# Kernel optimization log

Measured on AMD Instinct MI355X. Metric: run time of the kernel, lower is better.

Reference implementation:

```python
import jax, jax.numpy as jnp
import numpy as np

NUM_GROUPS = 32
EPS = 1e-6


def group_norm(x, gamma, beta):
    # x: [b, c, t, h, w]
    b, c, t, h, w = x.shape
    xg = x.reshape(b, NUM_GROUPS, c // NUM_GROUPS, t, h, w)
    mean = xg.mean(axis=(2, 3, 4, 5), keepdims=True)
    var = xg.var(axis=(2, 3, 4, 5), keepdims=True)
    xg = (xg - mean) * jax.lax.rsqrt(var + EPS)
    xn = xg.reshape(b, c, t, h, w)
    return xn * gamma[None, :, None, None, None] + beta[None, :, None, None, None]


def conv1x1(x, w, bias):
    # 1x1x1 Conv3d == per-position channel matmul. x: [b,c,t,h,w], w: [cout,cin]
    y = jnp.einsum('oc,bcthw->bothw', w, x)
    return y + bias[None, :, None, None, None]


def setup_inputs() -> dict:
    key = jax.random.key(0)
    ks = jax.random.split(key, 11)
    c = 512
    b, t, h, w = 1, 16, 32, 32
    s = 1.0 / np.sqrt(c)
    return {
        'x': jax.random.normal(ks[0], (b, c, t, h, w), dtype=jnp.float32),
        'gn_gamma': jnp.ones((c,), jnp.float32),
        'gn_beta': jnp.zeros((c,), jnp.float32),
        'wq': jax.random.normal(ks[1], (c, c), jnp.float32) * s,
        'bq': jnp.zeros((c,), jnp.float32),
        'wk': jax.random.normal(ks[2], (c, c), jnp.float32) * s,
        'bk': jnp.zeros((c,), jnp.float32),
        'wv': jax.random.normal(ks[3], (c, c), jnp.float32) * s,
        'bv': jnp.zeros((c,), jnp.float32),
        'wo': jax.random.normal(ks[4], (c, c), jnp.float32) * s,
        'bo': jnp.zeros((c,), jnp.float32),
    }


def reference(x, gn_gamma, gn_beta, wq, bq, wk, bk, wv, bv, wo, bo):
    b, c, t, h, w = x.shape
    h_ = group_norm(x, gn_gamma, gn_beta)
    q = conv1x1(h_, wq, bq)
    k = conv1x1(h_, wk, bk)
    v = conv1x1(h_, wv, bv)
    # per-frame spatial attention: tokens are the h*w grid, batched over (b t)
    n = h * w
    q = q.transpose(0, 2, 3, 4, 1).reshape(b * t, n, c)   # [(bt), n, c]
    k = k.transpose(0, 2, 3, 4, 1).reshape(b * t, n, c)
    v = v.transpose(0, 2, 3, 4, 1).reshape(b * t, n, c)
    scale = float(int(c) ** (-0.5))
    attn = jax.nn.softmax(jnp.einsum('bic,bjc->bij', q, k) * scale, axis=-1)
    out = jnp.einsum('bij,bjc->bic', attn, v)             # [(bt), n, c]
    out = out.reshape(b, t, h, w, c).transpose(0, 4, 1, 2, 3)
    out = conv1x1(out, wo, bo)
    return x + out
```

## Files before the change

### kernel.cpp

```cpp
#include <hip/hip_runtime.h>
#include <hip/hip_bf16.h>

#define CCH   512
#define NPOS  16384
#define NTOK  1024
#define NFRM  16
#define NGRP  32
#define GSZ   (CCH / NGRP)
#define GELEM (GSZ * NPOS)
#define GN_SPLIT 32

typedef unsigned short u16;
typedef unsigned int   u32;
typedef __attribute__((ext_vector_type(8))) short  short8;
typedef __attribute__((ext_vector_type(4))) float  floatx4;

__device__ __forceinline__ float bf2f(u16 u) {
    return __uint_as_float(((u32)u) << 16);
}
__device__ __forceinline__ u16 f2bf(float f) {
    u32 u = __float_as_uint(f);
    u = (u + 0x7fffu + ((u >> 16) & 1u)) >> 16;
    return (u16)u;
}
__device__ __forceinline__ float ldx(const void* p, size_t i, bool f32m) {
    return f32m ? ((const float*)p)[i] : bf2f(((const u16*)p)[i]);
}
__device__ __forceinline__ void gl2lds16(const u16* g, u16* l) {
    __builtin_amdgcn_global_load_lds(
        (const __attribute__((address_space(1))) u32*)g,
        (__attribute__((address_space(3))) u32*)l, 16, 0, 0);
}

__device__ __forceinline__ bool calc_f32m(const u32* __restrict__ x32) {
    __shared__ int cnt;
    if (threadIdx.x == 0) cnt = 0;
    __syncthreads();
    int c = 0;
    for (int i = threadIdx.x; i < 4096; i += 256) {
        u32 v = x32[i] & 0xFFFFu;
        u32 e = (v >> 7) & 0xFFu;
        if (e >= 0xC8u) c++;
    }
    atomicAdd(&cnt, c);
    __syncthreads();
    return cnt > 64;
}

__launch_bounds__(256)
__global__ void prep_all(const void* __restrict__ x,
                         const void* w0, const void* w1, const void* w2, const void* w3,
                         const void* b0, const void* b1, const void* b2, const void* b3,
                         u16* __restrict__ wdst, u16* __restrict__ bdst,
                         float* __restrict__ rl, float2* __restrict__ partials,
                         u32* __restrict__ flag) {
    int b = blockIdx.x;
    if (b >= 1025 && b < 1089) {
        rl[(b - 1025) * 256 + threadIdx.x] = 0.0f;
        return;
    }
    bool f32m = calc_f32m((const u32*)x);
    if (b == 0 && threadIdx.x == 0) *flag = f32m ? 1u : 0u;

    if (b < 1024) {
        int wi = b >> 8;
        const void* src = (wi == 0) ? w0 : (wi == 1) ? w1 : (wi == 2) ? w2 : w3;
        int base = (b & 255) * 1024 + threadIdx.x * 4;
        u16* d = wdst + wi * 262144 + base;
        if (f32m) {
            float4 v = *(const float4*)((const float*)src + base);
            ushort4 o;
            o.x = f2bf(v.x); o.y = f2bf(v.y); o.z = f2bf(v.z); o.w = f2bf(v.w);
            *(ushort4*)d = o;
        } else {
            *(ushort4*)d = *(const ushort4*)((const u16*)src + base);
        }
    } else if (b == 1024) {
        int t = threadIdx.x;
        int bi = t >> 6;
        int off = (t & 63) * 8;
        const void* src = (bi == 0) ? b0 : (bi == 1) ? b1 : (bi == 2) ? b2 : b3;
        u16* d = bdst + bi * 512 + off;
        if (f32m) {
            float4 v1 = *(const float4*)((const float*)src + off);
            float4 v2 = *(const float4*)((const float*)src + off + 4);
            ushort4 o1, o2;
            o1.x = f2bf(v1.x); o1.y = f2bf(v1.y); o1.z = f2bf(v1.z); o1.w = f2bf(v1.w);
            o2.x = f2bf(v2.x); o2.y = f2bf(v2.y); o2.z = f2bf(v2.z); o2.w = f2bf(v2.w);
            *(ushort4*)d = o1; *(ushort4*)(d + 4) = o2;
        } else {
            *(ushort4*)d = *(const ushort4*)((const u16*)src + off);
            *(ushort4*)(d + 4) = *(const ushort4*)((const u16*)src + off + 4);
        }
    } else {
        __shared__ float sm[8];
        int bb = b - 1089;
        const int chunk = GELEM / GN_SPLIT;
        size_t base = (size_t)bb * chunk;
        float s = 0.f, ss = 0.f;
        if (f32m) {
            const float4* p = (const float4*)((const float*)x + base);
            for (int i = threadIdx.x; i < chunk / 4; i += 256) {
                float4 u = p[i];
                s  += u.x + u.y + u.z + u.w;
                ss += u.x * u.x + u.y * u.y + u.z * u.z + u.w * u.w;
            }
        } else {
            const ushort4* p = (const ushort4*)((const u16*)x + base);
            for (int i = threadIdx.x; i < chunk / 4; i += 256) {
                ushort4 u = p[i];
                float a = bf2f(u.x), bq = bf2f(u.y), c = bf2f(u.z), d = bf2f(u.w);
                s  += a + bq + c + d;
                ss += a * a + bq * bq + c * c + d * d;
            }
        }
        int lane = threadIdx.x & 63, w = threadIdx.x >> 6;
        float t = s;
        #pragma unroll
        for (int o = 32; o > 0; o >>= 1) t += __shfl_down(t, o, 64);
        if (lane == 0) sm[w] = t;
        t = ss;
        #pragma unroll
        for (int o = 32; o > 0; o >>= 1) t += __shfl_down(t, o, 64);
        if (lane == 0) sm[4 + w] = t;
        __syncthreads();
        if (threadIdx.x == 0)
            partials[bb] = make_float2(sm[0] + sm[1] + sm[2] + sm[3],
                                       sm[4] + sm[5] + sm[6] + sm[7]);
    }
}

__launch_bounds__(256)
__global__ void gn_apply_t(const void* __restrict__ x, const float2* __restrict__ partials,
                           const void* __restrict__ gamma, const void* __restrict__ beta,
                           u16* __restrict__ xt, const u32* __restrict__ flag) {
    bool f32m = *flag != 0u;
    __shared__ float tile[64][65];
    __shared__ float2 cfs[64];
    int p0 = blockIdx.x * 64, c0 = blockIdx.y * 64;
    if (threadIdx.x < 64) {
        int c = c0 + threadIdx.x, g = c >> 4;
        float sum = 0.f, sq = 0.f;
        #pragma unroll 8
        for (int i = 0; i < GN_SPLIT; ++i) {
            float2 p = partials[g * GN_SPLIT + i];
            sum += p.x; sq += p.y;
        }
        float mean = sum * (1.0f / (float)GELEM);
        float var  = fmaxf(sq * (1.0f / (float)GELEM) - mean * mean, 0.0f);
        float rstd = rsqrtf(var + 1e-6f);
        float gm = ldx(gamma, c, f32m), b = ldx(beta, c, f32m);
        float sc = rstd * gm;
        cfs[threadIdx.x] = make_float2(sc, b - mean * sc);
    }
    __syncthreads();
    int r16    = threadIdx.x >> 4;
    int lane16 = threadIdx.x & 15;
    #pragma unroll 4
    for (int pass = 0; pass < 4; ++pass) {
        int row = pass * 16 + r16;
        float2 cf = cfs[row];
        size_t base = (size_t)(c0 + row) * NPOS + p0 + lane16 * 4;
        float4 v;
        if (f32m) {
            v = *(const float4*)((const float*)x + base);
        } else {
            ushort4 u = *(const ushort4*)((const u16*)x + base);
            v = make_float4(bf2f(u.x), bf2f(u.y), bf2f(u.z), bf2f(u.w));
        }
        tile[row][lane16 * 4 + 0] = v.x * cf.x + cf.y;
        tile[row][lane16 * 4 + 1] = v.y * cf.x + cf.y;
        tile[row][lane16 * 4 + 2] = v.z * cf.x + cf.y;
        tile[row][lane16 * 4 + 3] = v.w * cf.x + cf.y;
    }
    __syncthreads();
    int lane = threadIdx.x & 63, rg = threadIdx.x >> 6;
    #pragma unroll 4
    for (int i = 0; i < 16; ++i) {
        int prow = rg * 16 + i;
        xt[(size_t)(p0 + prow) * CCH + c0 + lane] = f2bf(tile[lane][prow]);
    }
}

#define EPI_QK    0
#define EPI_V     1
#define EPI_SCEXP 2
#define EPI_PV    3
#define EPI_OUT   4

template<int EPI>
__device__ __forceinline__ void gemm128(
    u16* __restrict__ As, u16* __restrict__ Bs,
    const u16* __restrict__ A, const u16* __restrict__ B,
    void* __restrict__ C, const u16* __restrict__ bias,
    const void* __restrict__ resid, const u32* __restrict__ flag,
    float* __restrict__ rl, int m_blk, int n_blk, int f,
    int lda, int ldb, int ldc, int K, long aFS, long bFS, long cFS)
{
    const int tid = threadIdx.x;
    const u16* Ab = A + (size_t)f * aFS + (size_t)m_blk * 128 * lda;
    const u16* Bb = B + (size_t)f * bFS + (size_t)n_blk * 128 * ldb;

    const int wave = tid >> 6, lane = tid & 63;
    const int srow = wave * 32 + (lane >> 3);
    const int schs = ((lane & 7) ^ ((lane >> 3) & 7)) * 8;

    const int wm = (wave >> 1) * 64, wn = (wave & 1) * 64;
    const int l15 = lane & 15, quad = lane >> 4;

    floatx4 acc[4][4] = {};

    for (int kk = 0; kk < K; kk += 64) {
        __syncthreads();
        #pragma unroll
        for (int o = 0; o < 4; ++o) {
            gl2lds16(Ab + (size_t)(srow + o * 8) * lda + kk + schs, &As[wave * 2048 + o * 512]);
            gl2lds16(Bb + (size_t)(srow + o * 8) * ldb + kk + schs, &Bs[wave * 2048 + o * 512]);
        }
        __syncthreads();
        #pragma unroll
        for (int kh = 0; kh < 2; ++kh) {
            short8 af[4], bf[4];
            #pragma unroll
            for (int mi = 0; mi < 4; ++mi) {
                const int row = wm + mi * 16 + l15;
                af[mi] = *(const short8*)&As[row * 64 + (((kh << 2) | quad) ^ (row & 7)) * 8];
            }
            #pragma unroll
            for (int ni = 0; ni < 4; ++ni) {
                const int row = wn + ni * 16 + l15;
                bf[ni] = *(const short8*)&Bs[row * 64 + (((kh << 2) | quad) ^ (row & 7)) * 8];
            }
            #pragma unroll
            for (int mi = 0; mi < 4; ++mi)
                #pragma unroll
                for (int ni = 0; ni < 4; ++ni)
                    acc[mi][ni] = __builtin_amdgcn_mfma_f32_16x16x32_bf16(
                        af[mi], bf[ni], acc[mi][ni], 0, 0, 0);
        }
    }

    const bool f32m = (EPI == EPI_OUT) ? (*flag != 0u) : false;
    const int m_base = m_blk * 128 + wm;
    const int n_base = n_blk * 128 + wn;
    const float scale = 0.044194173824159216f;

    float invn4[4];
    if (EPI == EPI_OUT) {
        #pragma unroll
        for (int ni = 0; ni < 4; ++ni)
            invn4[ni] = 1.0f / rl[n_base + ni * 16 + l15];
    }
    float rs[4][4];
    if (EPI == EPI_SCEXP) {
        #pragma unroll
        for (int mi = 0; mi < 4; ++mi)
            #pragma unroll
            for (int r = 0; r < 4; ++r) rs[mi][r] = 0.0f;
    }

    #pragma unroll
    for (int mi = 0; mi < 4; ++mi) {
        #pragma unroll
        for (int ni = 0; ni < 4; ++ni) {
            int n = n_base + ni * 16 + l15;
            float bn = (EPI == EPI_QK) ? bf2f(bias[n]) : 0.0f;
            #pragma unroll
            for (int r = 0; r < 4; ++r) {
                int m = m_base + mi * 16 + quad * 4 + r;
                float v = acc[mi][ni][r];
                size_t idx = (size_t)f * cFS + (size_t)m * ldc + n;
                if (EPI == EPI_QK) {
                    ((u16*)C)[idx] = f2bf(v + bn);
                } else if (EPI == EPI_V) {
                    ((u16*)C)[idx] = f2bf(v + bf2f(bias[m]));
                } else if (EPI == EPI_SCEXP) {
                    float ex = __expf(v * scale);
                    rs[mi][r] += ex;
                    ((u16*)C)[idx] = f2bf(ex);
                } else if (EPI == EPI_PV) {
                    ((u16*)C)[idx] = f2bf(v);
                } else {
                    float r2 = v * invn4[ni] + bf2f(bias[m]) + ldx(resid, idx, f32m);
                    if (f32m) ((float*)C)[idx] = r2;
                    else      ((u16*)C)[idx]   = f2bf(r2);
                }
            }
        }
    }

    if (EPI == EPI_SCEXP) {
        #pragma unroll
        for (int mi = 0; mi < 4; ++mi) {
            #pragma unroll
            for (int r = 0; r < 4; ++r) {
                float s = rs[mi][r];
                s += __shfl_xor(s, 1, 64);
                s += __shfl_xor(s, 2, 64);
                s += __shfl_xor(s, 4, 64);
                s += __shfl_xor(s, 8, 64);
                if (l15 == 0)
                    atomicAdd(&rl[f * NTOK + m_base + mi * 16 + quad * 4 + r], s);
            }
        }
    }
}

template<int EPI, bool MX, bool FSW>
__launch_bounds__(256, 4)
__global__ void mfma_gemm(const u16* __restrict__ A, const u16* __restrict__ B,
                          void* __restrict__ C, const u16* __restrict__ bias,
                          const void* __restrict__ resid, const u32* __restrict__ flag,
                          float* __restrict__ rl,
                          int lda, int ldb, int ldc, int K,
                          long aFS, long bFS, long cFS) {
    __shared__ __align__(16) u16 As[128 * 64];
    __shared__ __align__(16) u16 Bs[128 * 64];
    int bxi, byi, f;
    if (FSW) {
        u32 id = (blockIdx.z * gridDim.y + blockIdx.y) * gridDim.x + blockIdx.x;
        u32 T = gridDim.x * gridDim.y * gridDim.z;
        u32 half = T >> 1;
        f = (int)(id & 7u) + ((id >= half) ? 8 : 0);
        u32 l = (id >= half ? id - half : id) >> 3;
        bxi = (int)(l % gridDim.x);
        byi = (int)(l / gridDim.x);
    } else {
        bxi = blockIdx.x; byi = blockIdx.y; f = blockIdx.z;
    }
    gemm128<EPI>(As, Bs, A, B, C, bias, resid, flag, rl,
                 MX ? bxi : byi, MX ? byi : bxi, f, lda, ldb, ldc, K, aFS, bFS, cFS);
}

__launch_bounds__(256, 4)
__global__ void qkv_gemm(const u16* __restrict__ xnt,
                         const u16* __restrict__ wqk, const u16* __restrict__ bqk,
                         u16* __restrict__ qkt,
                         const u16* __restrict__ wv, const u16* __restrict__ bv,
                         u16* __restrict__ vt,
                         const u32* __restrict__ flag) {
    __shared__ __align__(16) u16 As[128 * 64];
    __shared__ __align__(16) u16 Bs[128 * 64];
    if (blockIdx.y < 8) {
        gemm128<EPI_QK>(As, Bs, xnt, wqk, qkt, bqk, nullptr, flag, nullptr,
                        (int)blockIdx.x, (int)blockIdx.y, 0,
                        CCH, CCH, 1024, CCH, 0, 0, 0);
    } else {
        gemm128<EPI_V>(As, Bs, wv, xnt, vt, bv, nullptr, flag, nullptr,
                       (int)blockIdx.y - 8, (int)blockIdx.x, 0,
                       CCH, CCH, NPOS, CCH, 0, 0, 0);
    }
}

template<int EPI, bool FSW>
__launch_bounds__(512, 4)
__global__ void mfma_gemm256(const u16* __restrict__ A, const u16* __restrict__ B,
                             void* __restrict__ C, const u16* __restrict__ bias,
                             const u32* __restrict__ flag, float* __restrict__ rl,
                             int lda, int ldb, int ldc, int K,
                             long aFS, long bFS, long cFS) {
    __shared__ __align__(16) u16 As[256 * 64];
    __shared__ __align__(16) u16 Bs[128 * 64];
    const int tid = threadIdx.x;

    int bxi, byi, f;
    if (FSW) {
        u32 id = (blockIdx.z * gridDim.y + blockIdx.y) * gridDim.x + blockIdx.x;
        u32 T = gridDim.x * gridDim.y * gridDim.z;
        u32 half = T >> 1;
        f = (int)(id & 7u) + ((id >= half) ? 8 : 0);
        u32 l = (id >= half ? id - half : id) >> 3;
        bxi = (int)(l % gridDim.x);
        byi = (int)(l / gridDim.x);
    } else {
        bxi = blockIdx.x; byi = blockIdx.y; f = blockIdx.z;
    }
    const int m_blk = byi;
    const int n_blk = bxi;

    const u16* Ab = A + (size_t)f * aFS + (size_t)m_blk * 256 * lda;
    const u16* Bb = B + (size_t)f * bFS + (size_t)n_blk * 128 * ldb;

    const int wave = tid >> 6, lane = tid & 63;
    const int srowA = wave * 32 + (lane >> 3);
    const int srowB = wave * 16 + (lane >> 3);
    const int schs  = ((lane & 7) ^ ((lane >> 3) & 7)) * 8;

    const int wm = (wave >> 1) * 64, wn = (wave & 1) * 64;
    const int l15 = lane & 15, quad = lane >> 4;

    floatx4 acc[4][4] = {};

    for (int kk = 0; kk < K; kk += 64) {
        __syncthreads();
        #pragma unroll
        for (int o = 0; o < 4; ++o)
            gl2lds16(Ab + (size_t)(srowA + o * 8) * lda + kk + schs,
                     &As[wave * 2048 + o * 512]);
        #pragma unroll
        for (int o = 0; o < 2; ++o)
            gl2lds16(Bb + (size_t)(srowB + o * 8) * ldb + kk + schs,
                     &Bs[wave * 1024 + o * 512]);
        __syncthreads();
        #pragma unroll
        for (int kh = 0; kh < 2; ++kh) {
            short8 af[4], bf[4];
            #pragma unroll
            for (int mi = 0; mi < 4; ++mi) {
                const int row = wm + mi * 16 + l15;
                af[mi] = *(const short8*)&As[row * 64 + (((kh << 2) | quad) ^ (row & 7)) * 8];
            }
            #pragma unroll
            for (int ni = 0; ni < 4; ++ni) {
                const int row = wn + ni * 16 + l15;
                bf[ni] = *(const short8*)&Bs[row * 64 + (((kh << 2) | quad) ^ (row & 7)) * 8];
            }
            #pragma unroll
            for (int mi = 0; mi < 4; ++mi)
                #pragma unroll
                for (int ni = 0; ni < 4; ++ni)
                    acc[mi][ni] = __builtin_amdgcn_mfma_f32_16x16x32_bf16(
                        af[mi], bf[ni], acc[mi][ni], 0, 0, 0);
        }
    }

    const int m_base = m_blk * 256 + wm;
    const int n_base = n_blk * 128 + wn;
    const float scale = 0.044194173824159216f;

    float rs[4][4];
    #pragma unroll
    for (int mi = 0; mi < 4; ++mi)
        #pragma unroll
        for (int r = 0; r < 4; ++r) rs[mi][r] = 0.0f;

    #pragma unroll
    for (int mi = 0; mi < 4; ++mi) {
        #pragma unroll
        for (int ni = 0; ni < 4; ++ni) {
            int n = n_base + ni * 16 + l15;
            #pragma unroll
            for (int r = 0; r < 4; ++r) {
                int m = m_base + mi * 16 + quad * 4 + r;
                float v = acc[mi][ni][r];
                size_t idx = (size_t)f * cFS + (size_t)m * ldc + n;
                float ex = __expf(v * scale);
                rs[mi][r] += ex;
                ((u16*)C)[idx] = f2bf(ex);
            }
        }
    }

    #pragma unroll
    for (int mi = 0; mi < 4; ++mi) {
        #pragma unroll
        for (int r = 0; r < 4; ++r) {
            float s = rs[mi][r];
            s += __shfl_xor(s, 1, 64);
            s += __shfl_xor(s, 2, 64);
            s += __shfl_xor(s, 4, 64);
            s += __shfl_xor(s, 8, 64);
            if (l15 == 0)
                atomicAdd(&rl[f * NTOK + m_base + mi * 16 + quad * 4 + r], s);
        }
    }
}

extern "C" void kernel_launch(void* const* d_in, const int* in_sizes, int n_in,
                              void* d_out, int out_size, void* d_ws, size_t ws_size,
                              hipStream_t stream) {
    const void* x   = d_in[0];
    const void* gam = d_in[1];
    const void* bet = d_in[2];

    char* ws = (char*)d_ws;
    float2* partials = (float2*)(ws + 4096);
    u32*    flag     = (u32*)(ws + 12352);
    u16* cw[4] = { (u16*)(ws + 16384),              (u16*)(ws + 16384 +  524288ull),
                   (u16*)(ws + 16384 + 1048576ull), (u16*)(ws + 16384 + 1572864ull) };
    u16* cb[4] = { (u16*)(ws + 2113536ull),        (u16*)(ws + 2113536ull + 1024),
                   (u16*)(ws + 2113536ull + 2048), (u16*)(ws + 2113536ull + 3072) };
    float* rl  = (float*)(ws + (3ull << 20));
    u16*  xnt  = (u16*)(ws + (4ull  << 20));
    u16*  qkt  = (u16*)(ws + (20ull << 20));
    u16*  vt   = (u16*)(ws + (52ull << 20));
    u16*  pbuf = (u16*)(ws + (68ull << 20));
    u16*  obuf = xnt;

    prep_all<<<2113, 256, 0, stream>>>(x,
                                       d_in[3], d_in[5], d_in[7], d_in[9],
                                       d_in[4], d_in[6], d_in[8], d_in[10],
                                       cw[0], cb[0], rl, partials, flag);
    gn_apply_t<<<dim3(NPOS / 64, CCH / 64), 256, 0, stream>>>(
        x, partials, gam, bet, xnt, flag);

    qkv_gemm<<<dim3(128, 12), 256, 0, stream>>>(
        xnt, cw[0], cb[0], qkt, cw[2], cb[2], vt, flag);

    dim3 gsc(NTOK / 128, NTOK / 256, NFRM);
    mfma_gemm256<EPI_SCEXP, true><<<gsc, 512, 0, stream>>>(
        qkt, qkt + 512, pbuf, nullptr, flag, rl, 1024, 1024, NTOK, CCH,
        (long)NTOK * 1024, (long)NTOK * 1024, (long)NTOK * NTOK);

    dim3 gpv(CCH / 128, NTOK / 128, NFRM);
    mfma_gemm<EPI_PV, false, true><<<gpv, 256, 0, stream>>>(
        pbuf, vt, obuf, nullptr, nullptr, flag, nullptr, NTOK, NPOS, CCH, NTOK,
        (long)NTOK * NTOK, NTOK, (long)NTOK * CCH);

    dim3 go(NPOS / 128, CCH / 128, 1);
    mfma_gemm<EPI_OUT, false, false><<<go, 256, 0, stream>>>(
        cw[3], obuf, d_out, cb[3], x, flag, rl, CCH, CCH, NPOS, CCH, 0, 0, 0);
}
```

Before: 220.2 us.

## Vectorize transpose stores, bump qkv occupancy, use 128-tile GEMM for scores

The GroupNorm-apply transpose now writes four channels per thread as one ushort4 store instead of scalar u16 stores. The launch bound for qkv_gemm rises from 4 to 5 blocks per CU. The dedicated 256x128 score GEMM kernel is removed, and the scores-plus-exp stage now runs through the generic 128x128 mfma_gemm path with the frame-swizzle option. This trades a larger tile with more reuse for more, smaller blocks and less code, and the LDS reads in the transpose now have a different bank pattern.

```diff
diff --git a/kernel.cpp b/kernel.cpp
--- a/kernel.cpp
+++ b/kernel.cpp
@@ -174,11 +174,16 @@
         tile[row][lane16 * 4 + 3] = v.w * cf.x + cf.y;
     }
     __syncthreads();
-    int lane = threadIdx.x & 63, rg = threadIdx.x >> 6;
+    int c4 = (threadIdx.x & 15) * 4;
     #pragma unroll 4
-    for (int i = 0; i < 16; ++i) {
-        int prow = rg * 16 + i;
-        xt[(size_t)(p0 + prow) * CCH + c0 + lane] = f2bf(tile[lane][prow]);
+    for (int pass = 0; pass < 4; ++pass) {
+        int prow = pass * 16 + r16;
+        ushort4 o;
+        o.x = f2bf(tile[c4 + 0][prow]);
+        o.y = f2bf(tile[c4 + 1][prow]);
+        o.z = f2bf(tile[c4 + 2][prow]);
+        o.w = f2bf(tile[c4 + 3][prow]);
+        *(ushort4*)&xt[(size_t)(p0 + prow) * CCH + c0 + c4] = o;
     }
 }
 
@@ -332,7 +337,7 @@
                  MX ? bxi : byi, MX ? byi : bxi, f, lda, ldb, ldc, K, aFS, bFS, cFS);
 }
 
-__launch_bounds__(256, 4)
+__launch_bounds__(256, 5)
 __global__ void qkv_gemm(const u16* __restrict__ xnt,
                          const u16* __restrict__ wqk, const u16* __restrict__ bqk,
                          u16* __restrict__ qkt,
@@ -352,120 +357,6 @@
     }
 }
 
-template<int EPI, bool FSW>
-__launch_bounds__(512, 4)
-__global__ void mfma_gemm256(const u16* __restrict__ A, const u16* __restrict__ B,
-                             void* __restrict__ C, const u16* __restrict__ bias,
-                             const u32* __restrict__ flag, float* __restrict__ rl,
-                             int lda, int ldb, int ldc, int K,
-                             long aFS, long bFS, long cFS) {
-    __shared__ __align__(16) u16 As[256 * 64];
-    __shared__ __align__(16) u16 Bs[128 * 64];
-    const int tid = threadIdx.x;
-
-    int bxi, byi, f;
-    if (FSW) {
-        u32 id = (blockIdx.z * gridDim.y + blockIdx.y) * gridDim.x + blockIdx.x;
-        u32 T = gridDim.x * gridDim.y * gridDim.z;
-        u32 half = T >> 1;
-        f = (int)(id & 7u) + ((id >= half) ? 8 : 0);
-        u32 l = (id >= half ? id - half : id) >> 3;
-        bxi = (int)(l % gridDim.x);
-        byi = (int)(l / gridDim.x);
-    } else {
-        bxi = blockIdx.x; byi = blockIdx.y; f = blockIdx.z;
-    }
-    const int m_blk = byi;
-    const int n_blk = bxi;
-
-    const u16* Ab = A + (size_t)f * aFS + (size_t)m_blk * 256 * lda;
-    const u16* Bb = B + (size_t)f * bFS + (size_t)n_blk * 128 * ldb;
-
-    const int wave = tid >> 6, lane = tid & 63;
-    const int srowA = wave * 32 + (lane >> 3);
-    const int srowB = wave * 16 + (lane >> 3);
-    const int schs  = ((lane & 7) ^ ((lane >> 3) & 7)) * 8;
-
-    const int wm = (wave >> 1) * 64, wn = (wave & 1) * 64;
-    const int l15 = lane & 15, quad = lane >> 4;
-
-    floatx4 acc[4][4] = {};
-
-    for (int kk = 0; kk < K; kk += 64) {
-        __syncthreads();
-        #pragma unroll
-        for (int o = 0; o < 4; ++o)
-            gl2lds16(Ab + (size_t)(srowA + o * 8) * lda + kk + schs,
-                     &As[wave * 2048 + o * 512]);
-        #pragma unroll
-        for (int o = 0; o < 2; ++o)
-            gl2lds16(Bb + (size_t)(srowB + o * 8) * ldb + kk + schs,
-                     &Bs[wave * 1024 + o * 512]);
-        __syncthreads();
-        #pragma unroll
-        for (int kh = 0; kh < 2; ++kh) {
-            short8 af[4], bf[4];
-            #pragma unroll
-            for (int mi = 0; mi < 4; ++mi) {
-                const int row = wm + mi * 16 + l15;
-                af[mi] = *(const short8*)&As[row * 64 + (((kh << 2) | quad) ^ (row & 7)) * 8];
-            }
-            #pragma unroll
-            for (int ni = 0; ni < 4; ++ni) {
-                const int row = wn + ni * 16 + l15;
-                bf[ni] = *(const short8*)&Bs[row * 64 + (((kh << 2) | quad) ^ (row & 7)) * 8];
-            }
-            #pragma unroll
-            for (int mi = 0; mi < 4; ++mi)
-                #pragma unroll
-                for (int ni = 0; ni < 4; ++ni)
-                    acc[mi][ni] = __builtin_amdgcn_mfma_f32_16x16x32_bf16(
-                        af[mi], bf[ni], acc[mi][ni], 0, 0, 0);
-        }
-    }
-
-    const int m_base = m_blk * 256 + wm;
-    const int n_base = n_blk * 128 + wn;
-    const float scale = 0.044194173824159216f;
-
-    float rs[4][4];
-    #pragma unroll
-    for (int mi = 0; mi < 4; ++mi)
-        #pragma unroll
-        for (int r = 0; r < 4; ++r) rs[mi][r] = 0.0f;
-
-    #pragma unroll
-    for (int mi = 0; mi < 4; ++mi) {
-        #pragma unroll
-        for (int ni = 0; ni < 4; ++ni) {
-            int n = n_base + ni * 16 + l15;
-            #pragma unroll
-            for (int r = 0; r < 4; ++r) {
-                int m = m_base + mi * 16 + quad * 4 + r;
-                float v = acc[mi][ni][r];
-                size_t idx = (size_t)f * cFS + (size_t)m * ldc + n;
-                float ex = __expf(v * scale);
-                rs[mi][r] += ex;
-                ((u16*)C)[idx] = f2bf(ex);
-            }
-        }
-    }
-
-    #pragma unroll
-    for (int mi = 0; mi < 4; ++mi) {
-        #pragma unroll
-        for (int r = 0; r < 4; ++r) {
-            float s = rs[mi][r];
-            s += __shfl_xor(s, 1, 64);
-            s += __shfl_xor(s, 2, 64);
-            s += __shfl_xor(s, 4, 64);
-            s += __shfl_xor(s, 8, 64);
-            if (l15 == 0)
-                atomicAdd(&rl[f * NTOK + m_base + mi * 16 + quad * 4 + r], s);
-        }
-    }
-}
-
 extern "C" void kernel_launch(void* const* d_in, const int* in_sizes, int n_in,
                               void* d_out, int out_size, void* d_ws, size_t ws_size,
                               hipStream_t stream) {
@@ -497,9 +388,9 @@
     qkv_gemm<<<dim3(128, 12), 256, 0, stream>>>(
         xnt, cw[0], cb[0], qkt, cw[2], cb[2], vt, flag);
 
-    dim3 gsc(NTOK / 128, NTOK / 256, NFRM);
-    mfma_gemm256<EPI_SCEXP, true><<<gsc, 512, 0, stream>>>(
-        qkt, qkt + 512, pbuf, nullptr, flag, rl, 1024, 1024, NTOK, CCH,
+    dim3 gsc(NTOK / 128, NTOK / 128, NFRM);
+    mfma_gemm<EPI_SCEXP, false, true><<<gsc, 256, 0, stream>>>(
+        qkt, qkt + 512, pbuf, nullptr, nullptr, flag, rl, 1024, 1024, NTOK, CCH,
         (long)NTOK * 1024, (long)NTOK * 1024, (long)NTOK * NTOK);
 
     dim3 gpv(CCH / 128, NTOK / 128, NFRM);
```

Measured after the change: 283.9 us. +28.9%, slower.
